# Performance work log

Hardware: AMD Instinct MI355X
Metric: run time of the kernel (lower is better)

Reference implementation:

```python
import jax, jax.numpy as jnp
import numpy as np

C = 64
R = 0.25
S = 32
CR = int(C * R)  # 16
EPS = 1e-5


def _bn(x, g, b, m, v):
    # x: [B, O, N], per-channel inference-mode BatchNorm1d
    inv = g / jnp.sqrt(v + EPS)
    return x * inv[None, :, None] + (b - m * inv)[None, :, None]


def _ln(x, g, b):
    mu = jnp.mean(x, axis=-1, keepdims=True)
    var = jnp.mean(jnp.square(x - mu), axis=-1, keepdims=True)
    return (x - mu) / jnp.sqrt(var + EPS) * g + b


def setup_inputs() -> dict:
    key = jax.random.key(0)
    ks = jax.random.split(key, 4)
    B, N = 8, 4096
    O1 = int(2 * C * R * C)  # 2048
    return {
        "pre_features": jax.random.normal(ks[0], (B, C, N, S), jnp.float32),
        "features": jax.random.normal(ks[1], (B, C, N), jnp.float32),
        "w1": jax.random.normal(ks[2], (O1, C), jnp.float32) * 0.05,
        "bn1_g": jnp.ones((O1,), jnp.float32),
        "bn1_b": jnp.zeros((O1,), jnp.float32),
        "bn1_m": jnp.zeros((O1,), jnp.float32),
        "bn1_v": jnp.ones((O1,), jnp.float32),
        "ln1_g": jnp.ones((CR,), jnp.float32),
        "ln1_b": jnp.zeros((CR,), jnp.float32),
        "ln2_g": jnp.ones((C,), jnp.float32),
        "ln2_b": jnp.zeros((C,), jnp.float32),
        "w2": jax.random.normal(ks[3], (C, C * S), jnp.float32) * 0.05,
        "bn2_g": jnp.ones((C,), jnp.float32),
        "bn2_b": jnp.zeros((C,), jnp.float32),
        "bn2_m": jnp.zeros((C,), jnp.float32),
        "bn2_v": jnp.ones((C,), jnp.float32),
    }


def reference(pre_features, features, w1, bn1_g, bn1_b, bn1_m, bn1_v,
              ln1_g, ln1_b, ln2_g, ln2_b, w2, bn2_g, bn2_b, bn2_m, bn2_v):
    B, _, N = features.shape
    # net1: 1x1 conv + BN + ReLU -> [B, 2*C^2*R, N]
    x = jnp.einsum('bcn,oc->bon', features, w1)
    x = jax.nn.relu(_bn(x, bn1_g, bn1_b, bn1_m, bn1_v))
    dyn = jnp.transpose(x, (0, 2, 1))  # [B, N, 2*C*CR]
    param1 = dyn[:, :, :C * CR].reshape(B, N, C, CR)
    param2 = dyn[:, :, C * CR:].reshape(B, N, CR, C)
    pre = jnp.transpose(pre_features, (0, 2, 3, 1))  # [B, N, S, C]
    t = jax.nn.relu(_ln(jnp.einsum('bnsc,bncr->bnsr', pre, param1), ln1_g, ln1_b))
    t = jax.nn.relu(_ln(jnp.einsum('bnsr,bnrc->bnsc', t, param2), ln2_g, ln2_b))
    flat = jnp.transpose(t.reshape(B, N, S * C), (0, 2, 1))  # [B, S*C, N]
    # net2: 1x1 conv + BN + ReLU
    y = jnp.einsum('bkn,ok->bon', flat, w2)
    y = jax.nn.relu(_bn(y, bn2_g, bn2_b, bn2_m, bn2_v))
    return jax.nn.relu(y + features)
```

## Files before the change

kernel.cpp:

```cpp
#include <hip/hip_runtime.h>
#include <hip/hip_bf16.h>

typedef __attribute__((ext_vector_type(8)))  short short8;
typedef __attribute__((ext_vector_type(4)))  float f32x4;
typedef __attribute__((ext_vector_type(16))) float f32x16;

constexpr float EPSf = 1e-5f;

__device__ __forceinline__ unsigned short f2bf(float f) {
    union { float f; unsigned int i; } x; x.f = f;
    unsigned int r = x.i + 0x7fffu + ((x.i >> 16) & 1u);
    return (unsigned short)(r >> 16);
}
__device__ __forceinline__ unsigned int pk2bf(float lo, float hi) {
    union { __hip_bfloat162 h; unsigned int u; } z;
    z.h = __float22bfloat162_rn(make_float2(lo, hi));
    return z.u;
}

__device__ __forceinline__ int P1a(int pt, int r, int c) {
    return pt*4096 + ((r*128 + c*2) ^ (((r ^ pt) & 7) << 4));
}
__device__ __forceinline__ int P2a(int pt, int c, int r) {
    return pt*4096 + 2048 + ((c*32 + r*2) ^ (((((c>>2)&1) ^ (pt&7))) << 4));
}
__device__ __forceinline__ int FTa(int pt, int k) {
    return pt*4096 + ((k*2) ^ (((pt ^ (k>>6)) & 7) << 4));
}
__device__ __forceinline__ int FBa(int pt, int c) {
    return 65536 + pt*128 + ((c*2) ^ ((pt&7) << 4));
}
__device__ __forceinline__ int T1a(int w, int s, int r) {
    return 65536 + w*1024 + ((s*32 + r*2) ^ (((s>>2)&1) << 4));
}
__device__ __forceinline__ int PARTw(int kh, int mt, int pt, int g) {
    return 65536 + ((kh*4 + mt) << 10) + pt*64 + ((g ^ ((pt>>1)&3)) << 4);
}
__device__ __forceinline__ int PARTr(int kh, int mt, int pt, int o16) {
    return 65536 + ((kh*4 + mt) << 10) + pt*64
         + ((((o16>>2) ^ ((pt>>1)&3)) << 4) | ((o16&3) << 2));
}

__global__ void prep_kernel(const float* __restrict__ w1,
                            const float* __restrict__ g1, const float* __restrict__ b1,
                            const float* __restrict__ m1, const float* __restrict__ v1,
                            const float* __restrict__ w2,
                            const float* __restrict__ g2, const float* __restrict__ b2,
                            const float* __restrict__ m2, const float* __restrict__ v2,
                            unsigned short* __restrict__ w1f, unsigned short* __restrict__ w2f,
                            float* __restrict__ sh1, float* __restrict__ sh2) {
    int idx = blockIdx.x * 256 + threadIdx.x;
    if (idx < 2048*64) {
        int o = idx >> 6, cin = idx & 63;
        float inv = g1[o] * rsqrtf(v1[o] + EPSf);
        int m;
        if (o < 1024) { m = (o & 15)*64 + (o >> 4); }
        else          { int o2 = o - 1024; m = 1024 + (o2 & 63)*16 + (o2 >> 6); }
        int i = m >> 4, row = m & 15;
        int kk = cin >> 5, gg = (cin >> 3) & 3, j = cin & 7;
        w1f[(((i*2 + kk)*64) + gg*16 + row)*8 + j] = f2bf(w1[idx] * inv);

        int o2w = idx >> 11, k = idx & 2047;
        float inv2 = g2[o2w] * rsqrtf(v2[o2w] + EPSf);
        int ks = k >> 5, mt = o2w >> 4, gk = (k >> 3) & 3, j2 = k & 7;
        w2f[(((ks*4 + mt)*64) + gk*16 + (o2w & 15))*8 + j2] = f2bf(w2[idx] * inv2);
    }
    if (idx < 2048) {
        int o = idx;
        float inv = g1[o] * rsqrtf(v1[o] + EPSf);
        float val = b1[o] - m1[o] * inv;
        int m;
        if (o < 1024) { m = (o & 15)*64 + (o >> 4); }
        else          { int o2 = o - 1024; m = 1024 + (o2 & 63)*16 + (o2 >> 6); }
        sh1[m] = val;
    }
    if (idx < 64) sh2[idx] = b2[idx] - m2[idx] * (g2[idx] * rsqrtf(v2[idx] + EPSf));
}

__global__ __launch_bounds__(512, 4) void dyn_mfma(
    const float* __restrict__ pre, const float* __restrict__ feat,
    const unsigned short* __restrict__ w1f, const unsigned short* __restrict__ w2f,
    const float* __restrict__ sh1, const float* __restrict__ sh2,
    const float* __restrict__ ln1g, const float* __restrict__ ln1b,
    const float* __restrict__ ln2g, const float* __restrict__ ln2b,
    float* __restrict__ out)
{
    __shared__ __align__(16) unsigned char smem[73728];
    unsigned short* sm16 = (unsigned short*)smem;

    const int tid = threadIdx.x;
    const int w  = tid >> 6, l = tid & 63;
    const int lr = l & 15, g = l >> 4;
    const int c32 = l & 31, hi = l >> 5;

    const int p0 = blockIdx.x * 16;
    const int b  = p0 >> 12, n0 = p0 & 4095;

    const f32x4 zz4 = {0.f, 0.f, 0.f, 0.f};
    const f32x16 zz16 = {};

    const float* pbase0 = pre + (size_t)b*8388608 + (size_t)(n0 + w*2 + 0)*32;
    const float* pbase1 = pbase0 + 32;
    float pf[2][2][8];
    #pragma unroll
    for (int kk = 0; kk < 2; ++kk)
        #pragma unroll
        for (int nt = 0; nt < 2; ++nt)
            #pragma unroll
            for (int j = 0; j < 8; ++j)
                pf[kk][nt][j] = pbase0[(size_t)(kk*32 + g*8 + j)*131072 + nt*16 + lr];

    {
        int c = tid >> 3, pj = tid & 7;
        const float* fb = feat + ((size_t)(b*64 + c))*4096 + n0 + pj;
        sm16[FBa(pj,     c) >> 1] = f2bf(fb[0]);
        sm16[FBa(pj + 8, c) >> 1] = f2bf(fb[8]);
    }

    short8 pb0[2][2], pb1[2][2];
    #pragma unroll
    for (int kk = 0; kk < 2; ++kk)
        #pragma unroll
        for (int nt = 0; nt < 2; ++nt) {
            union { unsigned int u[4]; short8 s; } z;
            #pragma unroll
            for (int d = 0; d < 4; ++d)
                z.u[d] = pk2bf(pf[kk][nt][2*d], pf[kk][nt][2*d + 1]);
            pb0[kk][nt] = z.s;
        }
    float pf1[2][2][8];
    #pragma unroll
    for (int kk = 0; kk < 2; ++kk)
        #pragma unroll
        for (int nt = 0; nt < 2; ++nt)
            #pragma unroll
            for (int j = 0; j < 8; ++j)
                pf1[kk][nt][j] = pbase1[(size_t)(kk*32 + g*8 + j)*131072 + nt*16 + lr];
    __syncthreads();

    {
        short8 bf0 = *(const short8*)&smem[FBa(lr, g*8)];
        short8 bf1 = *(const short8*)&smem[FBa(lr, 32 + g*8)];
        const unsigned short* w1p = w1f + ((size_t)(w*32)*64 + l)*8;
        #pragma unroll 8
        for (int ii = 0; ii < 16; ++ii) {
            short8 a0 = *(const short8*)(w1p + (ii*2 + 0)*512);
            short8 a1 = *(const short8*)(w1p + (ii*2 + 1)*512);
            f32x4 acc = __builtin_amdgcn_mfma_f32_16x16x32_bf16(a0, bf0, zz4, 0, 0, 0);
            acc = __builtin_amdgcn_mfma_f32_16x16x32_bf16(a1, bf1, acc, 0, 0, 0);
            const int i = w*16 + ii;
            f32x4 shv = *(const f32x4*)(sh1 + i*16 + g*4);
            float h0 = fmaxf(acc[0] + shv[0], 0.f);
            float h1 = fmaxf(acc[1] + shv[1], 0.f);
            float h2 = fmaxf(acc[2] + shv[2], 0.f);
            float h3 = fmaxf(acc[3] + shv[3], 0.f);
            uint2 hv; hv.x = pk2bf(h0, h1); hv.y = pk2bf(h2, h3);
            if (w < 4) {
                *(uint2*)&smem[P1a(lr, i >> 2, (i & 3)*16 + g*4)] = hv;
            } else {
                *(uint2*)&smem[P2a(lr, i - 64, g*4)] = hv;
            }
        }
    }
    #pragma unroll
    for (int kk = 0; kk < 2; ++kk)
        #pragma unroll
        for (int nt = 0; nt < 2; ++nt) {
            union { unsigned int u[4]; short8 s; } z;
            #pragma unroll
            for (int d = 0; d < 4; ++d)
                z.u[d] = pk2bf(pf1[kk][nt][2*d], pf1[kk][nt][2*d + 1]);
            pb1[kk][nt] = z.s;
        }
    __syncthreads();

    {
        f32x4 l1g = *(const f32x4*)(ln1g + g*4);
        f32x4 l1b = *(const f32x4*)(ln1b + g*4);
        auto stageB = [&](int pt, const short8 (&pbx)[2][2]) {
            short8 a1f0 = *(const short8*)&smem[P1a(pt, lr, g*8)];
            short8 a1f1 = *(const short8*)&smem[P1a(pt, lr, 32 + g*8)];
            f32x4 acc1[2];
            #pragma unroll
            for (int nt = 0; nt < 2; ++nt) {
                f32x4 a = __builtin_amdgcn_mfma_f32_16x16x32_bf16(a1f0, pbx[0][nt], zz4, 0, 0, 0);
                acc1[nt] = __builtin_amdgcn_mfma_f32_16x16x32_bf16(a1f1, pbx[1][nt], a, 0, 0, 0);
            }
            #pragma unroll
            for (int nt = 0; nt < 2; ++nt) {
                float s0 = acc1[nt][0] + acc1[nt][1] + acc1[nt][2] + acc1[nt][3];
                float q0 = acc1[nt][0]*acc1[nt][0] + acc1[nt][1]*acc1[nt][1]
                         + acc1[nt][2]*acc1[nt][2] + acc1[nt][3]*acc1[nt][3];
                s0 += __shfl_xor(s0, 16); s0 += __shfl_xor(s0, 32);
                q0 += __shfl_xor(q0, 16); q0 += __shfl_xor(q0, 32);
                float mu = s0 * 0.0625f;
                float rs = rsqrtf(q0 * 0.0625f - mu*mu + EPSf);
                float v0 = fmaxf((acc1[nt][0] - mu)*rs*l1g[0] + l1b[0], 0.f);
                float v1 = fmaxf((acc1[nt][1] - mu)*rs*l1g[1] + l1b[1], 0.f);
                float v2 = fmaxf((acc1[nt][2] - mu)*rs*l1g[2] + l1b[2], 0.f);
                float v3 = fmaxf((acc1[nt][3] - mu)*rs*l1g[3] + l1b[3], 0.f);
                uint2 dd; dd.x = pk2bf(v0, v1); dd.y = pk2bf(v2, v3);
                *(uint2*)&smem[T1a(w, nt*16 + lr, g*4)] = dd;
            }
            short8 bt1  = *(const short8*)&smem[T1a(w, c32, hi*8)];
            short8 a2f0 = *(const short8*)&smem[P2a(pt, c32, hi*8)];
            short8 a2f1 = *(const short8*)&smem[P2a(pt, 32 + c32, hi*8)];
            f32x16 acc2a = __builtin_amdgcn_mfma_f32_32x32x16_bf16(a2f0, bt1, zz16, 0, 0, 0);
            f32x16 acc2b = __builtin_amdgcn_mfma_f32_32x32x16_bf16(a2f1, bt1, zz16, 0, 0, 0);
            float sm2 = 0.f, sq2 = 0.f;
            #pragma unroll
            for (int e = 0; e < 16; ++e) { float v = acc2a[e]; sm2 += v; sq2 += v*v; }
            #pragma unroll
            for (int e = 0; e < 16; ++e) { float v = acc2b[e]; sm2 += v; sq2 += v*v; }
            sm2 += __shfl_xor(sm2, 32); sq2 += __shfl_xor(sq2, 32);
            float mu2 = sm2 * (1.0f/64.0f);
            float rs2 = rsqrtf(sq2 * (1.0f/64.0f) - mu2*mu2 + EPSf);
            #pragma unroll
            for (int qh = 0; qh < 4; ++qh) {
                int c0 = qh*8 + hi*4;
                f32x4 gq = *(const f32x4*)(ln2g + c0);
                f32x4 bq = *(const f32x4*)(ln2b + c0);
                float t0 = fmaxf((acc2a[qh*4 + 0] - mu2)*rs2*gq[0] + bq[0], 0.f);
                float t1 = fmaxf((acc2a[qh*4 + 1] - mu2)*rs2*gq[1] + bq[1], 0.f);
                float t2 = fmaxf((acc2a[qh*4 + 2] - mu2)*rs2*gq[2] + bq[2], 0.f);
                float t3 = fmaxf((acc2a[qh*4 + 3] - mu2)*rs2*gq[3] + bq[3], 0.f);
                uint2 dd; dd.x = pk2bf(t0, t1); dd.y = pk2bf(t2, t3);
                *(uint2*)&smem[FTa(pt, c32*64 + c0)] = dd;
            }
            #pragma unroll
            for (int qh = 0; qh < 4; ++qh) {
                int c0 = 32 + qh*8 + hi*4;
                f32x4 gq = *(const f32x4*)(ln2g + c0);
                f32x4 bq = *(const f32x4*)(ln2b + c0);
                float t0 = fmaxf((acc2b[qh*4 + 0] - mu2)*rs2*gq[0] + bq[0], 0.f);
                float t1 = fmaxf((acc2b[qh*4 + 1] - mu2)*rs2*gq[1] + bq[1], 0.f);
                float t2 = fmaxf((acc2b[qh*4 + 2] - mu2)*rs2*gq[2] + bq[2], 0.f);
                float t3 = fmaxf((acc2b[qh*4 + 3] - mu2)*rs2*gq[3] + bq[3], 0.f);
                uint2 dd; dd.x = pk2bf(t0, t1); dd.y = pk2bf(t2, t3);
                *(uint2*)&smem[FTa(pt, c32*64 + c0)] = dd;
            }
        };
        stageB(w*2 + 0, pb0);
        stageB(w*2 + 1, pb1);
    }
    __syncthreads();

    {
        const int kh = w >> 2, mt = w & 3;
        f32x4 acc = zz4;
        #pragma unroll 4
        for (int t = 0; t < 32; ++t) {
            const int ks = kh*32 + t;
            short8 bfl = *(const short8*)&smem[FTa(lr, ks*32 + g*8)];
            short8 af  = *(const short8*)(w2f + ((size_t)(ks*4 + mt)*64 + l)*8);
            acc = __builtin_amdgcn_mfma_f32_16x16x32_bf16(af, bfl, acc, 0, 0, 0);
        }
        *(f32x4*)&smem[PARTw(kh, mt, lr, g)] = acc;
    }
    __syncthreads();
    {
        const int ro = tid >> 3, rp = tid & 7;
        const int mt2 = ro >> 4, o16 = ro & 15;
        const float sh2v = sh2[ro];
        #pragma unroll
        for (int ph = 0; ph < 2; ++ph) {
            const int pt = rp + ph*8;
            float s = *(const float*)&smem[PARTr(0, mt2, pt, o16)]
                    + *(const float*)&smem[PARTr(1, mt2, pt, o16)];
            float y = fmaxf(s + sh2v, 0.f);
            size_t oidx = ((size_t)(b*64 + ro))*4096 + n0 + pt;
            out[oidx] = fmaxf(y + feat[oidx], 0.f);
        }
    }
}

extern "C" void kernel_launch(void* const* d_in, const int* in_sizes, int n_in,
                              void* d_out, int out_size, void* d_ws, size_t ws_size,
                              hipStream_t stream) {
    (void)in_sizes; (void)n_in; (void)out_size; (void)ws_size;
    const float* pre  = (const float*)d_in[0];
    const float* feat = (const float*)d_in[1];
    const float* w1   = (const float*)d_in[2];
    const float* bn1g = (const float*)d_in[3];
    const float* bn1b = (const float*)d_in[4];
    const float* bn1m = (const float*)d_in[5];
    const float* bn1v = (const float*)d_in[6];
    const float* ln1g = (const float*)d_in[7];
    const float* ln1b = (const float*)d_in[8];
    const float* ln2g = (const float*)d_in[9];
    const float* ln2b = (const float*)d_in[10];
    const float* w2   = (const float*)d_in[11];
    const float* bn2g = (const float*)d_in[12];
    const float* bn2b = (const float*)d_in[13];
    const float* bn2m = (const float*)d_in[14];
    const float* bn2v = (const float*)d_in[15];
    float* out = (float*)d_out;

    unsigned short* w1f = (unsigned short*)d_ws;
    unsigned short* w2f = w1f + 2048*64;
    float* sh1 = (float*)(w2f + 64*2048);
    float* sh2 = sh1 + 2048;

    prep_kernel<<<512, 256, 0, stream>>>(w1, bn1g, bn1b, bn1m, bn1v,
                                         w2, bn2g, bn2b, bn2m, bn2v,
                                         w1f, w2f, sh1, sh2);
    dyn_mfma<<<2048, 512, 0, stream>>>(pre, feat, w1f, w2f, sh1, sh2,
                                       ln1g, ln1b, ln2g, ln2b, out);
}
```

Baseline: 116.0 us.

## Make blocks persistent over four point tiles with prefetch of next tile inputs

Each block now processes 64 points in four 16-point iterations instead of one tile, cutting the grid from 2048 to 512 blocks. The next tile's features and pre_features loads are issued during the final GEMM of the current tile, so global load latency overlaps with compute. The final GEMM loop is split into two independent accumulators to shorten the MFMA dependency chain. The region used for T1 and the partial sums moves so it no longer overlaps the feature buffer, which enlarges shared memory. The fewer blocks and the extra shared memory and registers may lower occupancy and parallelism.

```diff
diff --git a/kernel.cpp b/kernel.cpp
--- a/kernel.cpp
+++ b/kernel.cpp
@@ -31,13 +31,13 @@
     return 65536 + pt*128 + ((c*2) ^ ((pt&7) << 4));
 }
 __device__ __forceinline__ int T1a(int w, int s, int r) {
-    return 65536 + w*1024 + ((s*32 + r*2) ^ (((s>>2)&1) << 4));
+    return 67584 + w*1024 + ((s*32 + r*2) ^ (((s>>2)&1) << 4));
 }
 __device__ __forceinline__ int PARTw(int kh, int mt, int pt, int g) {
-    return 65536 + ((kh*4 + mt) << 10) + pt*64 + ((g ^ ((pt>>1)&3)) << 4);
+    return 67584 + ((kh*4 + mt) << 10) + pt*64 + ((g ^ ((pt>>1)&3)) << 4);
 }
 __device__ __forceinline__ int PARTr(int kh, int mt, int pt, int o16) {
-    return 65536 + ((kh*4 + mt) << 10) + pt*64
+    return 67584 + ((kh*4 + mt) << 10) + pt*64
          + ((((o16>>2) ^ ((pt>>1)&3)) << 4) | ((o16&3) << 2));
 }
 
@@ -85,7 +85,7 @@
     const float* __restrict__ ln2g, const float* __restrict__ ln2b,
     float* __restrict__ out)
 {
-    __shared__ __align__(16) unsigned char smem[73728];
+    __shared__ __align__(16) unsigned char smem[75776];
     unsigned short* sm16 = (unsigned short*)smem;
 
     const int tid = threadIdx.x;
@@ -93,183 +93,202 @@
     const int lr = l & 15, g = l >> 4;
     const int c32 = l & 31, hi = l >> 5;
 
-    const int p0 = blockIdx.x * 16;
-    const int b  = p0 >> 12, n0 = p0 & 4095;
+    const int base_pt = blockIdx.x * 64;
+    const int b = base_pt >> 12;
 
     const f32x4 zz4 = {0.f, 0.f, 0.f, 0.f};
     const f32x16 zz16 = {};
 
-    const float* pbase0 = pre + (size_t)b*8388608 + (size_t)(n0 + w*2 + 0)*32;
-    const float* pbase1 = pbase0 + 32;
-    float pf[2][2][8];
-    #pragma unroll
-    for (int kk = 0; kk < 2; ++kk)
+    float fb0, fb1;
+    float pf0[2][2][8];
+
+    const unsigned short* w1p = w1f + ((size_t)(w*32)*64 + l)*8;
+    f32x4 l1g = *(const f32x4*)(ln1g + g*4);
+    f32x4 l1b = *(const f32x4*)(ln1b + g*4);
+
+    auto issue_next = [&](int n0x) {
+        const float* fbp = feat + ((size_t)(b*64 + (tid >> 3)))*4096 + n0x + (tid & 7);
+        fb0 = fbp[0];
+        fb1 = fbp[8];
+        const float* pbn = pre + (size_t)b*8388608 + (size_t)(n0x + w*2)*32;
         #pragma unroll
-        for (int nt = 0; nt < 2; ++nt)
-            #pragma unroll
-            for (int j = 0; j < 8; ++j)
-                pf[kk][nt][j] = pbase0[(size_t)(kk*32 + g*8 + j)*131072 + nt*16 + lr];
-
-    {
-        int c = tid >> 3, pj = tid & 7;
-        const float* fb = feat + ((size_t)(b*64 + c))*4096 + n0 + pj;
-        sm16[FBa(pj,     c) >> 1] = f2bf(fb[0]);
-        sm16[FBa(pj + 8, c) >> 1] = f2bf(fb[8]);
-    }
-
-    short8 pb0[2][2], pb1[2][2];
-    #pragma unroll
-    for (int kk = 0; kk < 2; ++kk)
+        for (int kk = 0; kk < 2; ++kk)
+            #pragma unroll
+            for (int nt = 0; nt < 2; ++nt)
+                #pragma unroll
+                for (int j = 0; j < 8; ++j)
+                    pf0[kk][nt][j] = pbn[(size_t)(kk*32 + g*8 + j)*131072 + nt*16 + lr];
+    };
+
+    issue_next(base_pt & 4095);
+
+    #pragma unroll 1
+    for (int it = 0; it < 4; ++it) {
+        const int n0 = (base_pt & 4095) + it*16;
+
+        {
+            int c = tid >> 3, pj = tid & 7;
+            sm16[FBa(pj,     c) >> 1] = f2bf(fb0);
+            sm16[FBa(pj + 8, c) >> 1] = f2bf(fb1);
+        }
+        short8 pb0[2][2], pb1[2][2];
         #pragma unroll
-        for (int nt = 0; nt < 2; ++nt) {
-            union { unsigned int u[4]; short8 s; } z;
-            #pragma unroll
-            for (int d = 0; d < 4; ++d)
-                z.u[d] = pk2bf(pf[kk][nt][2*d], pf[kk][nt][2*d + 1]);
-            pb0[kk][nt] = z.s;
-        }
-    float pf1[2][2][8];
-    #pragma unroll
-    for (int kk = 0; kk < 2; ++kk)
+        for (int kk = 0; kk < 2; ++kk)
+            #pragma unroll
+            for (int nt = 0; nt < 2; ++nt) {
+                union { unsigned int u[4]; short8 s; } z;
+                #pragma unroll
+                for (int d = 0; d < 4; ++d)
+                    z.u[d] = pk2bf(pf0[kk][nt][2*d], pf0[kk][nt][2*d + 1]);
+                pb0[kk][nt] = z.s;
+            }
+        const float* pbase1 = pre + (size_t)b*8388608 + (size_t)(n0 + w*2 + 1)*32;
+        float pf1[2][2][8];
         #pragma unroll
-        for (int nt = 0; nt < 2; ++nt)
-            #pragma unroll
-            for (int j = 0; j < 8; ++j)
-                pf1[kk][nt][j] = pbase1[(size_t)(kk*32 + g*8 + j)*131072 + nt*16 + lr];
-    __syncthreads();
-
-    {
-        short8 bf0 = *(const short8*)&smem[FBa(lr, g*8)];
-        short8 bf1 = *(const short8*)&smem[FBa(lr, 32 + g*8)];
-        const unsigned short* w1p = w1f + ((size_t)(w*32)*64 + l)*8;
-        #pragma unroll 8
-        for (int ii = 0; ii < 16; ++ii) {
-            short8 a0 = *(const short8*)(w1p + (ii*2 + 0)*512);
-            short8 a1 = *(const short8*)(w1p + (ii*2 + 1)*512);
-            f32x4 acc = __builtin_amdgcn_mfma_f32_16x16x32_bf16(a0, bf0, zz4, 0, 0, 0);
-            acc = __builtin_amdgcn_mfma_f32_16x16x32_bf16(a1, bf1, acc, 0, 0, 0);
-            const int i = w*16 + ii;
-            f32x4 shv = *(const f32x4*)(sh1 + i*16 + g*4);
-            float h0 = fmaxf(acc[0] + shv[0], 0.f);
-            float h1 = fmaxf(acc[1] + shv[1], 0.f);
-            float h2 = fmaxf(acc[2] + shv[2], 0.f);
-            float h3 = fmaxf(acc[3] + shv[3], 0.f);
-            uint2 hv; hv.x = pk2bf(h0, h1); hv.y = pk2bf(h2, h3);
-            if (w < 4) {
-                *(uint2*)&smem[P1a(lr, i >> 2, (i & 3)*16 + g*4)] = hv;
-            } else {
-                *(uint2*)&smem[P2a(lr, i - 64, g*4)] = hv;
-            }
-        }
-    }
-    #pragma unroll
-    for (int kk = 0; kk < 2; ++kk)
+        for (int kk = 0; kk < 2; ++kk)
+            #pragma unroll
+            for (int nt = 0; nt < 2; ++nt)
+                #pragma unroll
+                for (int j = 0; j < 8; ++j)
+                    pf1[kk][nt][j] = pbase1[(size_t)(kk*32 + g*8 + j)*131072 + nt*16 + lr];
+        __syncthreads();
+
+        {
+            short8 bf0 = *(const short8*)&smem[FBa(lr, g*8)];
+            short8 bf1 = *(const short8*)&smem[FBa(lr, 32 + g*8)];
+            #pragma unroll 8
+            for (int ii = 0; ii < 16; ++ii) {
+                short8 a0 = *(const short8*)(w1p + (ii*2 + 0)*512);
+                short8 a1 = *(const short8*)(w1p + (ii*2 + 1)*512);
+                f32x4 acc = __builtin_amdgcn_mfma_f32_16x16x32_bf16(a0, bf0, zz4, 0, 0, 0);
+                acc = __builtin_amdgcn_mfma_f32_16x16x32_bf16(a1, bf1, acc, 0, 0, 0);
+                const int i = w*16 + ii;
+                f32x4 shv = *(const f32x4*)(sh1 + i*16 + g*4);
+                float h0 = fmaxf(acc[0] + shv[0], 0.f);
+                float h1 = fmaxf(acc[1] + shv[1], 0.f);
+                float h2 = fmaxf(acc[2] + shv[2], 0.f);
+                float h3 = fmaxf(acc[3] + shv[3], 0.f);
+                uint2 hv; hv.x = pk2bf(h0, h1); hv.y = pk2bf(h2, h3);
+                if (w < 4) {
+                    *(uint2*)&smem[P1a(lr, i >> 2, (i & 3)*16 + g*4)] = hv;
+                } else {
+                    *(uint2*)&smem[P2a(lr, i - 64, g*4)] = hv;
+                }
+            }
+        }
         #pragma unroll
-        for (int nt = 0; nt < 2; ++nt) {
-            union { unsigned int u[4]; short8 s; } z;
-            #pragma unroll
-            for (int d = 0; d < 4; ++d)
-                z.u[d] = pk2bf(pf1[kk][nt][2*d], pf1[kk][nt][2*d + 1]);
-            pb1[kk][nt] = z.s;
-        }
-    __syncthreads();
-
-    {
-        f32x4 l1g = *(const f32x4*)(ln1g + g*4);
-        f32x4 l1b = *(const f32x4*)(ln1b + g*4);
-        auto stageB = [&](int pt, const short8 (&pbx)[2][2]) {
-            short8 a1f0 = *(const short8*)&smem[P1a(pt, lr, g*8)];
-            short8 a1f1 = *(const short8*)&smem[P1a(pt, lr, 32 + g*8)];
-            f32x4 acc1[2];
+        for (int kk = 0; kk < 2; ++kk)
             #pragma unroll
             for (int nt = 0; nt < 2; ++nt) {
-                f32x4 a = __builtin_amdgcn_mfma_f32_16x16x32_bf16(a1f0, pbx[0][nt], zz4, 0, 0, 0);
-                acc1[nt] = __builtin_amdgcn_mfma_f32_16x16x32_bf16(a1f1, pbx[1][nt], a, 0, 0, 0);
-            }
-            #pragma unroll
-            for (int nt = 0; nt < 2; ++nt) {
-                float s0 = acc1[nt][0] + acc1[nt][1] + acc1[nt][2] + acc1[nt][3];
-                float q0 = acc1[nt][0]*acc1[nt][0] + acc1[nt][1]*acc1[nt][1]
-                         + acc1[nt][2]*acc1[nt][2] + acc1[nt][3]*acc1[nt][3];
-                s0 += __shfl_xor(s0, 16); s0 += __shfl_xor(s0, 32);
-                q0 += __shfl_xor(q0, 16); q0 += __shfl_xor(q0, 32);
-                float mu = s0 * 0.0625f;
-                float rs = rsqrtf(q0 * 0.0625f - mu*mu + EPSf);
-                float v0 = fmaxf((acc1[nt][0] - mu)*rs*l1g[0] + l1b[0], 0.f);
-                float v1 = fmaxf((acc1[nt][1] - mu)*rs*l1g[1] + l1b[1], 0.f);
-                float v2 = fmaxf((acc1[nt][2] - mu)*rs*l1g[2] + l1b[2], 0.f);
-                float v3 = fmaxf((acc1[nt][3] - mu)*rs*l1g[3] + l1b[3], 0.f);
-                uint2 dd; dd.x = pk2bf(v0, v1); dd.y = pk2bf(v2, v3);
-                *(uint2*)&smem[T1a(w, nt*16 + lr, g*4)] = dd;
-            }
-            short8 bt1  = *(const short8*)&smem[T1a(w, c32, hi*8)];
-            short8 a2f0 = *(const short8*)&smem[P2a(pt, c32, hi*8)];
-            short8 a2f1 = *(const short8*)&smem[P2a(pt, 32 + c32, hi*8)];
-            f32x16 acc2a = __builtin_amdgcn_mfma_f32_32x32x16_bf16(a2f0, bt1, zz16, 0, 0, 0);
-            f32x16 acc2b = __builtin_amdgcn_mfma_f32_32x32x16_bf16(a2f1, bt1, zz16, 0, 0, 0);
-            float sm2 = 0.f, sq2 = 0.f;
-            #pragma unroll
-            for (int e = 0; e < 16; ++e) { float v = acc2a[e]; sm2 += v; sq2 += v*v; }
-            #pragma unroll
-            for (int e = 0; e < 16; ++e) { float v = acc2b[e]; sm2 += v; sq2 += v*v; }
-            sm2 += __shfl_xor(sm2, 32); sq2 += __shfl_xor(sq2, 32);
-            float mu2 = sm2 * (1.0f/64.0f);
-            float rs2 = rsqrtf(sq2 * (1.0f/64.0f) - mu2*mu2 + EPSf);
-            #pragma unroll
-            for (int qh = 0; qh < 4; ++qh) {
-                int c0 = qh*8 + hi*4;
-                f32x4 gq = *(const f32x4*)(ln2g + c0);
-                f32x4 bq = *(const f32x4*)(ln2b + c0);
-                float t0 = fmaxf((acc2a[qh*4 + 0] - mu2)*rs2*gq[0] + bq[0], 0.f);
-                float t1 = fmaxf((acc2a[qh*4 + 1] - mu2)*rs2*gq[1] + bq[1], 0.f);
-                float t2 = fmaxf((acc2a[qh*4 + 2] - mu2)*rs2*gq[2] + bq[2], 0.f);
-                float t3 = fmaxf((acc2a[qh*4 + 3] - mu2)*rs2*gq[3] + bq[3], 0.f);
-                uint2 dd; dd.x = pk2bf(t0, t1); dd.y = pk2bf(t2, t3);
-                *(uint2*)&smem[FTa(pt, c32*64 + c0)] = dd;
-            }
-            #pragma unroll
-            for (int qh = 0; qh < 4; ++qh) {
-                int c0 = 32 + qh*8 + hi*4;
-                f32x4 gq = *(const f32x4*)(ln2g + c0);
-                f32x4 bq = *(const f32x4*)(ln2b + c0);
-                float t0 = fmaxf((acc2b[qh*4 + 0] - mu2)*rs2*gq[0] + bq[0], 0.f);
-                float t1 = fmaxf((acc2b[qh*4 + 1] - mu2)*rs2*gq[1] + bq[1], 0.f);
-                float t2 = fmaxf((acc2b[qh*4 + 2] - mu2)*rs2*gq[2] + bq[2], 0.f);
-                float t3 = fmaxf((acc2b[qh*4 + 3] - mu2)*rs2*gq[3] + bq[3], 0.f);
-                uint2 dd; dd.x = pk2bf(t0, t1); dd.y = pk2bf(t2, t3);
-                *(uint2*)&smem[FTa(pt, c32*64 + c0)] = dd;
-            }
-        };
-        stageB(w*2 + 0, pb0);
-        stageB(w*2 + 1, pb1);
-    }
-    __syncthreads();
-
-    {
-        const int kh = w >> 2, mt = w & 3;
-        f32x4 acc = zz4;
-        #pragma unroll 4
-        for (int t = 0; t < 32; ++t) {
-            const int ks = kh*32 + t;
-            short8 bfl = *(const short8*)&smem[FTa(lr, ks*32 + g*8)];
-            short8 af  = *(const short8*)(w2f + ((size_t)(ks*4 + mt)*64 + l)*8);
-            acc = __builtin_amdgcn_mfma_f32_16x16x32_bf16(af, bfl, acc, 0, 0, 0);
-        }
-        *(f32x4*)&smem[PARTw(kh, mt, lr, g)] = acc;
-    }
-    __syncthreads();
-    {
-        const int ro = tid >> 3, rp = tid & 7;
-        const int mt2 = ro >> 4, o16 = ro & 15;
-        const float sh2v = sh2[ro];
-        #pragma unroll
-        for (int ph = 0; ph < 2; ++ph) {
-            const int pt = rp + ph*8;
-            float s = *(const float*)&smem[PARTr(0, mt2, pt, o16)]
-                    + *(const float*)&smem[PARTr(1, mt2, pt, o16)];
-            float y = fmaxf(s + sh2v, 0.f);
-            size_t oidx = ((size_t)(b*64 + ro))*4096 + n0 + pt;
-            out[oidx] = fmaxf(y + feat[oidx], 0.f);
+                union { unsigned int u[4]; short8 s; } z;
+                #pragma unroll
+                for (int d = 0; d < 4; ++d)
+                    z.u[d] = pk2bf(pf1[kk][nt][2*d], pf1[kk][nt][2*d + 1]);
+                pb1[kk][nt] = z.s;
+            }
+        __syncthreads();
+
+        {
+            auto stageB = [&](int pt, const short8 (&pbx)[2][2]) {
+                short8 a1f0 = *(const short8*)&smem[P1a(pt, lr, g*8)];
+                short8 a1f1 = *(const short8*)&smem[P1a(pt, lr, 32 + g*8)];
+                f32x4 acc1[2];
+                #pragma unroll
+                for (int nt = 0; nt < 2; ++nt) {
+                    f32x4 a = __builtin_amdgcn_mfma_f32_16x16x32_bf16(a1f0, pbx[0][nt], zz4, 0, 0, 0);
+                    acc1[nt] = __builtin_amdgcn_mfma_f32_16x16x32_bf16(a1f1, pbx[1][nt], a, 0, 0, 0);
+                }
+                #pragma unroll
+                for (int nt = 0; nt < 2; ++nt) {
+                    float s0 = acc1[nt][0] + acc1[nt][1] + acc1[nt][2] + acc1[nt][3];
+                    float q0 = acc1[nt][0]*acc1[nt][0] + acc1[nt][1]*acc1[nt][1]
+                             + acc1[nt][2]*acc1[nt][2] + acc1[nt][3]*acc1[nt][3];
+                    s0 += __shfl_xor(s0, 16); s0 += __shfl_xor(s0, 32);
+                    q0 += __shfl_xor(q0, 16); q0 += __shfl_xor(q0, 32);
+                    float mu = s0 * 0.0625f;
+                    float rs = rsqrtf(q0 * 0.0625f - mu*mu + EPSf);
+                    float v0 = fmaxf((acc1[nt][0] - mu)*rs*l1g[0] + l1b[0], 0.f);
+                    float v1 = fmaxf((acc1[nt][1] - mu)*rs*l1g[1] + l1b[1], 0.f);
+                    float v2 = fmaxf((acc1[nt][2] - mu)*rs*l1g[2] + l1b[2], 0.f);
+                    float v3 = fmaxf((acc1[nt][3] - mu)*rs*l1g[3] + l1b[3], 0.f);
+                    uint2 dd; dd.x = pk2bf(v0, v1); dd.y = pk2bf(v2, v3);
+                    *(uint2*)&smem[T1a(w, nt*16 + lr, g*4)] = dd;
+                }
+                short8 bt1  = *(const short8*)&smem[T1a(w, c32, hi*8)];
+                short8 a2f0 = *(const short8*)&smem[P2a(pt, c32, hi*8)];
+                short8 a2f1 = *(const short8*)&smem[P2a(pt, 32 + c32, hi*8)];
+                f32x16 acc2a = __builtin_amdgcn_mfma_f32_32x32x16_bf16(a2f0, bt1, zz16, 0, 0, 0);
+                f32x16 acc2b = __builtin_amdgcn_mfma_f32_32x32x16_bf16(a2f1, bt1, zz16, 0, 0, 0);
+                float sm2 = 0.f, sq2 = 0.f;
+                #pragma unroll
+                for (int e = 0; e < 16; ++e) { float v = acc2a[e]; sm2 += v; sq2 += v*v; }
+                #pragma unroll
+                for (int e = 0; e < 16; ++e) { float v = acc2b[e]; sm2 += v; sq2 += v*v; }
+                sm2 += __shfl_xor(sm2, 32); sq2 += __shfl_xor(sq2, 32);
+                float mu2 = sm2 * (1.0f/64.0f);
+                float rs2 = rsqrtf(sq2 * (1.0f/64.0f) - mu2*mu2 + EPSf);
+                #pragma unroll
+                for (int qh = 0; qh < 4; ++qh) {
+                    int c0 = qh*8 + hi*4;
+                    f32x4 gq = *(const f32x4*)(ln2g + c0);
+                    f32x4 bq = *(const f32x4*)(ln2b + c0);
+                    float t0 = fmaxf((acc2a[qh*4 + 0] - mu2)*rs2*gq[0] + bq[0], 0.f);
+                    float t1 = fmaxf((acc2a[qh*4 + 1] - mu2)*rs2*gq[1] + bq[1], 0.f);
+                    float t2 = fmaxf((acc2a[qh*4 + 2] - mu2)*rs2*gq[2] + bq[2], 0.f);
+                    float t3 = fmaxf((acc2a[qh*4 + 3] - mu2)*rs2*gq[3] + bq[3], 0.f);
+                    uint2 dd; dd.x = pk2bf(t0, t1); dd.y = pk2bf(t2, t3);
+                    *(uint2*)&smem[FTa(pt, c32*64 + c0)] = dd;
+                }
+                #pragma unroll
+                for (int qh = 0; qh < 4; ++qh) {
+                    int c0 = 32 + qh*8 + hi*4;
+                    f32x4 gq = *(const f32x4*)(ln2g + c0);
+                    f32x4 bq = *(const f32x4*)(ln2b + c0);
+                    float t0 = fmaxf((acc2b[qh*4 + 0] - mu2)*rs2*gq[0] + bq[0], 0.f);
+                    float t1 = fmaxf((acc2b[qh*4 + 1] - mu2)*rs2*gq[1] + bq[1], 0.f);
+                    float t2 = fmaxf((acc2b[qh*4 + 2] - mu2)*rs2*gq[2] + bq[2], 0.f);
+                    float t3 = fmaxf((acc2b[qh*4 + 3] - mu2)*rs2*gq[3] + bq[3], 0.f);
+                    uint2 dd; dd.x = pk2bf(t0, t1); dd.y = pk2bf(t2, t3);
+                    *(uint2*)&smem[FTa(pt, c32*64 + c0)] = dd;
+                }
+            };
+            stageB(w*2 + 0, pb0);
+            stageB(w*2 + 1, pb1);
+        }
+        __syncthreads();
+
+        {
+            const int kh = w >> 2, mt = w & 3;
+            f32x4 accA = zz4, accB = zz4;
+            #pragma unroll 4
+            for (int t = 0; t < 32; t += 2) {
+                const int ks = kh*32 + t;
+                short8 bfl0 = *(const short8*)&smem[FTa(lr, ks*32 + g*8)];
+                short8 af0  = *(const short8*)(w2f + ((size_t)(ks*4 + mt)*64 + l)*8);
+                short8 bfl1 = *(const short8*)&smem[FTa(lr, (ks+1)*32 + g*8)];
+                short8 af1  = *(const short8*)(w2f + ((size_t)((ks+1)*4 + mt)*64 + l)*8);
+                accA = __builtin_amdgcn_mfma_f32_16x16x32_bf16(af0, bfl0, accA, 0, 0, 0);
+                accB = __builtin_amdgcn_mfma_f32_16x16x32_bf16(af1, bfl1, accB, 0, 0, 0);
+            }
+            if (it < 3) issue_next(n0 + 16);
+            f32x4 acc = accA + accB;
+            *(f32x4*)&smem[PARTw(kh, mt, lr, g)] = acc;
+        }
+        __syncthreads();
+
+        {
+            const int ro = tid >> 3, rp = tid & 7;
+            const int mt2 = ro >> 4, o16 = ro & 15;
+            const float sh2v = sh2[ro];
+            #pragma unroll
+            for (int ph = 0; ph < 2; ++ph) {
+                const int pt = rp + ph*8;
+                float s = *(const float*)&smem[PARTr(0, mt2, pt, o16)]
+                        + *(const float*)&smem[PARTr(1, mt2, pt, o16)];
+                float y = fmaxf(s + sh2v, 0.f);
+                size_t oidx = ((size_t)(b*64 + ro))*4096 + n0 + pt;
+                out[oidx] = fmaxf(y + feat[oidx], 0.f);
+            }
         }
     }
 }
@@ -304,6 +323,6 @@
     prep_kernel<<<512, 256, 0, stream>>>(w1, bn1g, bn1b, bn1m, bn1v,
                                          w2, bn2g, bn2b, bn2m, bn2v,
                                          w1f, w2f, sh1, sh2);
-    dyn_mfma<<<2048, 512, 0, stream>>>(pre, feat, w1f, w2f, sh1, sh2,
-                                       ln1g, ln1b, ln2g, ln2b, out);
-}
+    dyn_mfma<<<512, 512, 0, stream>>>(pre, feat, w1f, w2f, sh1, sh2,
+                                      ln1g, ln1b, ln2g, ln2b, out);
+}
```

Result: slower. 425.1 us (+266.6%).
